# Kernel tuning notes

Measured on AMD Instinct MI355X. Metric: run time of the kernel, lower is better.

The kernel has to match this reference:

```python
import jax, jax.numpy as jnp
import numpy as np

NUM_HEADS = 8
NUM_GROUPS = 32
EPS = 1e-5


def setup_inputs() -> dict:
    key = jax.random.key(0)
    ks = jax.random.split(key, 7)
    B, C, H, W = 16, 512, 32, 32
    x = jax.random.normal(ks[0], (B, C, H, W), dtype=jnp.float32)
    gn_gamma = jnp.ones((C,), dtype=jnp.float32)
    gn_beta = jnp.zeros((C,), dtype=jnp.float32)
    # Conv1d with kernel_size=1 is a per-position matmul: weight [out, in]
    qkv_w = jax.random.normal(ks[1], (3 * C, C), dtype=jnp.float32) / np.sqrt(C)
    qkv_b = jax.random.normal(ks[2], (3 * C,), dtype=jnp.float32) * 0.01
    proj_w = jax.random.normal(ks[3], (C, C), dtype=jnp.float32) / np.sqrt(C)
    proj_b = jax.random.normal(ks[4], (C,), dtype=jnp.float32) * 0.01
    return {"x": x, "gn_gamma": gn_gamma, "gn_beta": gn_beta,
            "qkv_w": qkv_w, "qkv_b": qkv_b, "proj_w": proj_w, "proj_b": proj_b}


def group_norm(x, gamma, beta):
    # x: [B, C, H, W]
    B, C, H, W = x.shape
    xg = x.reshape(B, NUM_GROUPS, C // NUM_GROUPS, H, W)
    mean = xg.mean(axis=(2, 3, 4), keepdims=True)
    var = xg.var(axis=(2, 3, 4), keepdims=True)
    xg = (xg - mean) * jax.lax.rsqrt(var + EPS)
    x = xg.reshape(B, C, H, W)
    return x * gamma[None, :, None, None] + beta[None, :, None, None]


def reference(x, gn_gamma, gn_beta, qkv_w, qkv_b, proj_w, proj_b):
    B, C, H, W = x.shape
    N = H * W
    hd = C // NUM_HEADS  # head dim
    h = group_norm(x, gn_gamma, gn_beta).reshape(B, C, N)
    # 1x1 Conv1d == matmul over channel dim
    qkv = jnp.einsum('oc,bcn->bon', qkv_w, h) + qkv_b[None, :, None]
    qkv = qkv.reshape(B, 3, NUM_HEADS, hd, N)
    q, k, v = qkv[:, 0], qkv[:, 1], qkv[:, 2]  # each [B, h, d, N]
    scale = hd ** (-0.5)
    attn = jnp.einsum('bhdn,bhdm->bhnm', q, k) * scale  # [B, h, N, N]
    attn = jax.nn.softmax(attn, axis=-1)
    out = jnp.einsum('bhnm,bhdm->bhdn', attn, v).reshape(B, C, N)
    out = jnp.einsum('oc,bcn->bon', proj_w, out) + proj_b[None, :, None]
    return x + out.reshape(B, C, H, W)
```

## Files before the change

### kernel.cpp

```cpp
#include <hip/hip_runtime.h>

typedef unsigned short u16;
typedef unsigned int u32;
typedef __bf16 bf16x8 __attribute__((ext_vector_type(8)));
typedef float f32x4 __attribute__((ext_vector_type(4)));
typedef float f32x16 __attribute__((ext_vector_type(16)));

#define B_ 16
#define C_ 512
#define N_ 1024
#define NB_ 16384
#define K_ 512
#define M3_ 1536
#define SCALE_Q 0.18033688011112042f

__device__ __forceinline__ u16 f2bf(float f) {
  u32 u = __float_as_uint(f);
  u32 r = (u + 0x7FFFu + ((u >> 16) & 1u)) >> 16;
  return (u16)r;
}

__device__ __forceinline__ void gl_lds16(const void* g, void* l) {
  __builtin_amdgcn_global_load_lds(
      (const __attribute__((address_space(1))) u32*)(uintptr_t)g,
      (__attribute__((address_space(3))) u32*)(u32)(uintptr_t)l, 16, 0, 0);
}

__device__ __forceinline__ u32 cvtpk(float lo, float hi) {
  u32 r;
  asm("v_cvt_pk_bf16_f32 %0, %1, %2" : "=v"(r) : "v"(lo), "v"(hi));
  return r;
}

__device__ __forceinline__ float exp2a(float x) {
  float r;
  asm("v_exp_f32 %0, %1" : "=v"(r) : "v"(x));
  return r;
}

__device__ __forceinline__ void plswap2(u32& a, u32& b) {
#if __has_builtin(__builtin_amdgcn_permlane32_swap)
  auto r = __builtin_amdgcn_permlane32_swap((int)a, (int)b, false, false);
  a = (u32)r[0];
  b = (u32)r[1];
#else
  asm("v_permlane32_swap_b32 %0, %1" : "+v"(a), "+v"(b));
#endif
}

__device__ __forceinline__ float xhalf_sum(float x) {
  u32 a = __float_as_uint(x), b = a;
  plswap2(a, b);
  return __uint_as_float(a) + __uint_as_float(b);
}

__global__ __launch_bounds__(256) void cast2_kernel(const float* __restrict__ a,
                                                    const float* __restrict__ b,
                                                    u16* __restrict__ da,
                                                    u16* __restrict__ db,
                                                    int na, int nb) {
  int i = blockIdx.x * 256 + threadIdx.x;
  if (i < na) {
    da[i] = f2bf(a[i]);
  } else {
    int j = i - na;
    if (j < nb) db[j] = f2bf(b[j]);
  }
}

__global__ __launch_bounds__(256) void gnorm_kernel(const float* __restrict__ x,
                                                    const float* __restrict__ gamma,
                                                    const float* __restrict__ beta,
                                                    u16* __restrict__ ht) {
  int blk = blockIdx.x;
  int b = blk >> 5, g = blk & 31;
  int t = threadIdx.x;
  const float* xb = x + ((size_t)(b * C_ + g * 16) << 10);
  float v[16][4];
  float s = 0.f, sq = 0.f;
#pragma unroll
  for (int cc = 0; cc < 16; ++cc) {
#pragma unroll
    for (int r = 0; r < 4; ++r) {
      float f = xb[cc * 1024 + r * 256 + t];
      v[cc][r] = f; s += f; sq += f * f;
    }
  }
#pragma unroll
  for (int m = 32; m >= 1; m >>= 1) { s += __shfl_xor(s, m, 64); sq += __shfl_xor(sq, m, 64); }
  __shared__ float red[8];
  int w = t >> 6;
  if ((t & 63) == 0) { red[w * 2] = s; red[w * 2 + 1] = sq; }
  __syncthreads();
  s = red[0] + red[2] + red[4] + red[6];
  sq = red[1] + red[3] + red[5] + red[7];
  float mean = s * (1.f / 16384.f);
  float var = sq * (1.f / 16384.f) - mean * mean;
  float rstd = rsqrtf(var + 1e-5f);
  float gm[16], bt[16];
#pragma unroll
  for (int cc = 0; cc < 16; ++cc) {
    gm[cc] = gamma[g * 16 + cc] * rstd;
    bt[cc] = beta[g * 16 + cc];
  }
  u16* hb = ht + ((size_t)(b << 10)) * C_ + g * 16;
#pragma unroll
  for (int r = 0; r < 4; ++r) {
    u32 pk[8];
#pragma unroll
    for (int q = 0; q < 8; ++q) {
      float f0 = (v[2 * q][r] - mean) * gm[2 * q] + bt[2 * q];
      float f1 = (v[2 * q + 1][r] - mean) * gm[2 * q + 1] + bt[2 * q + 1];
      pk[q] = (u32)f2bf(f0) | ((u32)f2bf(f1) << 16);
    }
    u16* dp = hb + (size_t)(r * 256 + t) * C_;
    uint4 a = {pk[0], pk[1], pk[2], pk[3]};
    uint4 b4 = {pk[4], pk[5], pk[6], pk[7]};
    *(uint4*)dp = a;
    *(uint4*)(dp + 8) = b4;
  }
}

template <int EPI>
__global__ __launch_bounds__(256) void gemm_kernel(const u16* __restrict__ A,
                                                   const u16* __restrict__ BT,
                                                   const float* __restrict__ bias,
                                                   u16* __restrict__ Co,
                                                   u16* __restrict__ qTo,
                                                   u16* __restrict__ kTo,
                                                   const float* __restrict__ xres,
                                                   float* __restrict__ Fo) {
  __shared__ __attribute__((aligned(16))) u16 lds[4][8192];
  int t = threadIdx.x;
  int l = t & 63, w = t >> 6;
  int wr = w >> 1, wc = w & 1;
  int lid = blockIdx.y * 128 + blockIdx.x;
  int xcd = lid & 7, j2 = lid >> 3;
  int bx = xcd * 16 + (j2 & 15);
  int by = j2 >> 4;
  int ro0 = by * 128, co0 = bx * 128;
  f32x4 acc[4][4];
#pragma unroll
  for (int m = 0; m < 4; ++m)
#pragma unroll
    for (int n = 0; n < 4; ++n) acc[m][n] = {0.f, 0.f, 0.f, 0.f};

  int gsrc = ((l & 3) ^ ((l >> 3) & 3)) * 8;
  const u16* sA0 = A + (size_t)(ro0 + 2 * w * 16 + (l >> 2)) * K_ + gsrc;
  const u16* sA1 = sA0 + (size_t)16 * K_;
  const u16* sB0 = BT + (size_t)(co0 + 2 * w * 16 + (l >> 2)) * K_ + gsrc;
  const u16* sB1 = sB0 + (size_t)16 * K_;
  u32 dA0 = (2 * w) * 512, dA1 = (2 * w + 1) * 512;
  u32 dB0 = 4096 + (2 * w) * 512, dB1 = 4096 + (2 * w + 1) * 512;

  auto stage = [&](int hb) {
    u16* base = &lds[hb][0];
    gl_lds16(sA0, base + dA0);
    gl_lds16(sA1, base + dA1);
    gl_lds16(sB0, base + dB0);
    gl_lds16(sB1, base + dB1);
    sA0 += 32; sA1 += 32; sB0 += 32; sB1 += 32;
  };

  u32 slot = (((l >> 4) ^ (l >> 1)) & 3) * 8;
  u32 aro = (wr * 64 + (l & 15)) * 32 + slot;
  u32 bro = 4096 + (wc * 64 + (l & 15)) * 32 + slot;

  auto compute = [&](int hb) {
    const u16* base = &lds[hb][0];
    bf16x8 af[4], bfr[4];
#pragma unroll
    for (int m = 0; m < 4; ++m) af[m] = *(const bf16x8*)(base + aro + m * 512);
#pragma unroll
    for (int n = 0; n < 4; ++n) bfr[n] = *(const bf16x8*)(base + bro + n * 512);
    __builtin_amdgcn_s_setprio(1);
#pragma unroll
    for (int m = 0; m < 4; ++m)
#pragma unroll
      for (int n = 0; n < 4; ++n)
        acc[m][n] = __builtin_amdgcn_mfma_f32_16x16x32_bf16(af[m], bfr[n], acc[m][n], 0, 0, 0);
    __builtin_amdgcn_s_setprio(0);
  };

#define PHASE_SYNC(N)                                    \
  asm volatile("s_waitcnt vmcnt(" #N ")" ::: "memory"); \
  __builtin_amdgcn_sched_barrier(0);                     \
  __builtin_amdgcn_s_barrier();                          \
  __builtin_amdgcn_sched_barrier(0);

  stage(0);
  stage(1);
  stage(2);
#pragma unroll 1
  for (int h = 0; h < 13; ++h) {
    PHASE_SYNC(8)
    stage((h + 3) & 3);
    compute(h & 3);
  }
  PHASE_SYNC(8)
  compute(1);
  PHASE_SYNC(4)
  compute(2);
  PHASE_SYNC(0)
  compute(3);
#undef PHASE_SYNC

  if (EPI == 0 && ro0 < 1024) {
    int sel = ro0 >> 9;
    u16* dstb = sel ? kTo : qTo;
    float scl = sel ? 1.f : SCALE_Q;
#pragma unroll
    for (int m = 0; m < 4; ++m) {
      int row0 = ro0 + wr * 64 + m * 16 + (l >> 4) * 4;
      int o = row0 & 511;
      int h2 = o >> 6, d0 = o & 63;
      float bv0 = bias[row0], bv1 = bias[row0 + 1];
      float bv2 = bias[row0 + 2], bv3 = bias[row0 + 3];
#pragma unroll
      for (int n = 0; n < 4; ++n) {
        int col = co0 + wc * 64 + n * 16 + (l & 15);
        int bb = col >> 10, nn = col & 1023;
        float v0 = (acc[m][n][0] + bv0) * scl;
        float v1 = (acc[m][n][1] + bv1) * scl;
        float v2 = (acc[m][n][2] + bv2) * scl;
        float v3 = (acc[m][n][3] + bv3) * scl;
        uint2 ov = {cvtpk(v0, v1), cvtpk(v2, v3)};
        *(uint2*)(dstb + ((size_t)((bb * 8 + h2) << 10) + nn) * 64 + d0) = ov;
      }
    }
  } else {
#pragma unroll
    for (int m = 0; m < 4; ++m) {
#pragma unroll
      for (int j = 0; j < 4; ++j) {
        int row = ro0 + wr * 64 + m * 16 + (l >> 4) * 4 + j;
        float bv = bias[row];
#pragma unroll
        for (int n = 0; n < 4; ++n) {
          int col = co0 + wc * 64 + n * 16 + (l & 15);
          float val = acc[m][n][j] + bv;
          if (EPI == 0) {
            Co[(size_t)row * NB_ + col] = f2bf(val);
          } else {
            int bb = col >> 10, nn = col & 1023;
            size_t oi = (((size_t)(bb * C_ + row)) << 10) + nn;
            Fo[oi] = xres[oi] + val;
          }
        }
      }
    }
  }
}

__global__ __launch_bounds__(256) void attn_kernel(const u16* __restrict__ qT,
                                                   const u16* __restrict__ kT,
                                                   const u16* __restrict__ qkv,
                                                   u16* __restrict__ aoT) {
  __shared__ u16 KV[3][4096];
  int bid = blockIdx.x;
  int wid = (bid & 7) * 128 + (bid >> 3);
  int qt2 = wid & 7, h = (wid >> 3) & 7, b = wid >> 6;
  int bh = b * 8 + h;
  int t = threadIdx.x, l = t & 63, w = t >> 6;
  int lq = l & 31, hi = l >> 5;
  int q0 = qt2 * 128 + w * 32;

  const u16* qbase = qT + ((size_t)(bh << 10) + q0 + lq) * 64 + hi * 8;
  bf16x8 qf[4];
#pragma unroll
  for (int kc = 0; kc < 4; ++kc) qf[kc] = *(const bf16x8*)(qbase + kc * 16);

  f32x16 accO[2];
#pragma unroll
  for (int dt = 0; dt < 2; ++dt)
#pragma unroll
    for (int r = 0; r < 16; ++r) accO[dt][r] = 0.f;
  float lsum = 0.f;

  const u16 *src0, *src1;
  u32 ldso0, ldso1;
  int adv;
  if (w < 2) {
    int i0 = 2 * w, i1 = 2 * w + 1;
    src0 = kT + ((size_t)(bh << 10) + i0 * 8 + (l >> 3)) * 64 + (((l & 7) ^ ((l >> 3) & 7)) * 8);
    src1 = kT + ((size_t)(bh << 10) + i1 * 8 + (l >> 3)) * 64 + (((l & 7) ^ ((l >> 3) & 7)) * 8);
    ldso0 = i0 * 512; ldso1 = i1 * 512;
    adv = 2048;
  } else {
    int j0 = 2 * (w - 2), j1 = 2 * (w - 2) + 1;
    src0 = qkv + (size_t)(2 * C_ + h * 64 + j0 * 16 + (l >> 2)) * NB_ + (b << 10) +
           (((l & 3) ^ ((l >> 3) & 3)) * 8);
    src1 = qkv + (size_t)(2 * C_ + h * 64 + j1 * 16 + (l >> 2)) * NB_ + (b << 10) +
           (((l & 3) ^ ((l >> 3) & 3)) * 8);
    ldso0 = 2048 + j0 * 512; ldso1 = 2048 + j1 * 512;
    adv = 32;
  }

  u32 kfo[4], vfo[4];
#pragma unroll
  for (int kc = 0; kc < 4; ++kc)
    kfo[kc] = lq * 64 + (((2 * kc + hi) ^ (lq & 7)) * 8);
#pragma unroll
  for (int dt = 0; dt < 2; ++dt)
#pragma unroll
    for (int kcc = 0; kcc < 2; ++kcc)
      vfo[dt * 2 + kcc] = 2048 + (dt * 32 + lq) * 32 + (((kcc * 2 + hi) ^ ((lq >> 1) & 3)) * 8);

  auto stageTo = [&](u16* buf) {
    gl_lds16(src0, buf + ldso0);
    gl_lds16(src1, buf + ldso1);
    src0 += adv;
    src1 += adv;
  };

  auto qk = [&](const u16* buf, f32x16& sc) {
    bf16x8 kf[4];
#pragma unroll
    for (int kc = 0; kc < 4; ++kc) kf[kc] = *(const bf16x8*)(buf + kfo[kc]);
#pragma unroll
    for (int r = 0; r < 16; ++r) sc[r] = 0.f;
    __builtin_amdgcn_s_setprio(1);
#pragma unroll
    for (int kc = 0; kc < 4; ++kc)
      sc = __builtin_amdgcn_mfma_f32_32x32x16_bf16(kf[kc], qf[kc], sc, 0, 0, 0);
    __builtin_amdgcn_s_setprio(0);
  };

  auto finish = [&](const u16* buf, f32x16& sc) {
    bf16x8 vf[4];
#pragma unroll
    for (int j = 0; j < 4; ++j) vf[j] = *(const bf16x8*)(buf + vfo[j]);
    float p0 = 0.f, p1 = 0.f, p2 = 0.f, p3 = 0.f;
#pragma unroll
    for (int r = 0; r < 4; ++r) {
      float e0 = exp2a(sc[4 * r + 0]);
      float e1 = exp2a(sc[4 * r + 1]);
      float e2 = exp2a(sc[4 * r + 2]);
      float e3 = exp2a(sc[4 * r + 3]);
      sc[4 * r + 0] = e0; sc[4 * r + 1] = e1;
      sc[4 * r + 2] = e2; sc[4 * r + 3] = e3;
      p0 += e0; p1 += e1; p2 += e2; p3 += e3;
    }
    lsum += (p0 + p1) + (p2 + p3);
    u32 pk[8];
#pragma unroll
    for (int p = 0; p < 8; ++p) pk[p] = cvtpk(sc[2 * p], sc[2 * p + 1]);
    u32 pfu[2][4];
#pragma unroll
    for (int cc = 0; cc < 2; ++cc) {
      u32 w0 = pk[cc * 4 + 0], w2 = pk[cc * 4 + 2];
      u32 w1 = pk[cc * 4 + 1], w3 = pk[cc * 4 + 3];
      plswap2(w0, w2);
      plswap2(w1, w3);
      pfu[cc][0] = w0; pfu[cc][1] = w1; pfu[cc][2] = w2; pfu[cc][3] = w3;
    }
    __builtin_amdgcn_s_setprio(1);
#pragma unroll
    for (int kcc = 0; kcc < 2; ++kcc)
#pragma unroll
      for (int dt = 0; dt < 2; ++dt) {
        union { u32 u[4]; bf16x8 v; } pf;
        pf.u[0] = pfu[kcc][0]; pf.u[1] = pfu[kcc][1];
        pf.u[2] = pfu[kcc][2]; pf.u[3] = pfu[kcc][3];
        accO[dt] = __builtin_amdgcn_mfma_f32_32x32x16_bf16(vf[dt * 2 + kcc], pf.v, accO[dt], 0, 0, 0);
      }
    __builtin_amdgcn_s_setprio(0);
  };

#define WAITBAR(N)                                       \
  asm volatile("s_waitcnt vmcnt(" #N ")" ::: "memory"); \
  __builtin_amdgcn_sched_barrier(0);                     \
  __builtin_amdgcn_s_barrier();                          \
  __builtin_amdgcn_sched_barrier(0);

  u16* pa = &KV[0][0];
  u16* pb = &KV[1][0];
  u16* pc = &KV[2][0];
  f32x16 scA, scB;

  stageTo(pa);
  stageTo(pb);
  WAITBAR(0)
  qk(pa, scA);

#pragma unroll 1
  for (int s = 0; s < 15; ++s) {
    WAITBAR(0)
    stageTo(pc);
    qk(pb, scB);
    finish(pa, scA);
    u16* tp = pa; pa = pb; pb = pc; pc = tp;
    WAITBAR(0)
    stageTo(pc);
    qk(pb, scA);
    finish(pa, scB);
    tp = pa; pa = pb; pb = pc; pc = tp;
  }
  WAITBAR(0)
  qk(pb, scB);
  finish(pa, scA);
  pa = pb;
  finish(pa, scB);
#undef WAITBAR

  float inv = 1.0f / xhalf_sum(lsum);
  u16* ob = aoT + ((size_t)((b << 10) + q0 + lq)) * C_ + h * 64;
#pragma unroll
  for (int dt = 0; dt < 2; ++dt)
#pragma unroll
    for (int rg = 0; rg < 4; ++rg) {
      int d0 = dt * 32 + rg * 8 + hi * 4;
      u32 w0 = cvtpk(accO[dt][rg * 4 + 0] * inv, accO[dt][rg * 4 + 1] * inv);
      u32 w1 = cvtpk(accO[dt][rg * 4 + 2] * inv, accO[dt][rg * 4 + 3] * inv);
      uint2 o = {w0, w1};
      *(uint2*)(ob + d0) = o;
    }
}

extern "C" void kernel_launch(void* const* d_in, const int* in_sizes, int n_in,
                              void* d_out, int out_size, void* d_ws, size_t ws_size,
                              hipStream_t stream) {
  const float* x = (const float*)d_in[0];
  const float* gamma = (const float*)d_in[1];
  const float* beta = (const float*)d_in[2];
  const float* qkv_w = (const float*)d_in[3];
  const float* qkv_b = (const float*)d_in[4];
  const float* proj_w = (const float*)d_in[5];
  const float* proj_b = (const float*)d_in[6];
  float* out = (float*)d_out;
  char* ws = (char*)d_ws;
  u16* wq = (u16*)(ws);
  u16* wp = (u16*)(ws + 1572864);
  u16* ht = (u16*)(ws + 2097152);
  u16* qkvo = (u16*)(ws + 18874368);
  u16* qT = (u16*)(ws + 69206016);
  u16* kT = (u16*)(ws + 85983232);
  u16* aoT = ht;

  cast2_kernel<<<4096, 256, 0, stream>>>(qkv_w, proj_w, wq, wp, M3_ * K_, C_ * K_);
  gnorm_kernel<<<512, 256, 0, stream>>>(x, gamma, beta, ht);
  gemm_kernel<0><<<dim3(128, 12), 256, 0, stream>>>(wq, ht, qkv_b, qkvo, qT, kT, nullptr, nullptr);
  attn_kernel<<<1024, 256, 0, stream>>>(qT, kT, qkvo, aoT);
  gemm_kernel<1><<<dim3(128, 4), 256, 0, stream>>>(wp, aoT, proj_b, nullptr, nullptr, nullptr, x, out);
}
```

Before: 123.9 us.

## Add dedicated QKV GEMM kernel with 128x256 tiles and triple-buffered LDS

Replaces the generic GEMM template for the QKV projection with a specialized kernel using a wider 128x256 output tile per block (64x12 grid instead of 128x12), so each B-operand load is reused across more rows. It uses a three-stage LDS ring with global_load_lds prefetch two stages ahead, synchronized with vmcnt waits and barriers. The larger tile raises register pressure (32 accumulator vectors per thread) and halves the block count, which may lower occupancy and wave-level parallelism.

After: 127.8 us. 3.2% more time.

```diff
diff --git a/kernel.cpp b/kernel.cpp
--- a/kernel.cpp
+++ b/kernel.cpp
@@ -118,6 +118,128 @@
     uint4 b4 = {pk[4], pk[5], pk[6], pk[7]};
     *(uint4*)dp = a;
     *(uint4*)(dp + 8) = b4;
+  }
+}
+
+__global__ __launch_bounds__(256) void gemm_qkv_kernel(const u16* __restrict__ A,
+                                                       const u16* __restrict__ BT,
+                                                       const float* __restrict__ bias,
+                                                       u16* __restrict__ Co,
+                                                       u16* __restrict__ qTo,
+                                                       u16* __restrict__ kTo) {
+  __shared__ __attribute__((aligned(16))) u16 lds[3][12288];
+  int t = threadIdx.x;
+  int l = t & 63, w = t >> 6;
+  int wr = w >> 1, wc = w & 1;
+  int lid = blockIdx.y * 64 + blockIdx.x;
+  int xcd = lid & 7, j2 = lid >> 3;
+  int bx = xcd * 8 + (j2 & 7);
+  int by = j2 >> 3;
+  int ro0 = by * 128, co0 = bx * 256;
+  f32x4 acc[4][8];
+#pragma unroll
+  for (int m = 0; m < 4; ++m)
+#pragma unroll
+    for (int n = 0; n < 8; ++n) acc[m][n] = {0.f, 0.f, 0.f, 0.f};
+
+  int gsrc = ((l & 3) ^ ((l >> 3) & 3)) * 8;
+  const u16* sA0 = A + (size_t)(ro0 + 32 * w + (l >> 2)) * K_ + gsrc;
+  const u16* sA1 = sA0 + (size_t)16 * K_;
+  const u16* sB0 = BT + (size_t)(co0 + 64 * w + (l >> 2)) * K_ + gsrc;
+  const u16* sB1 = sB0 + (size_t)16 * K_;
+  const u16* sB2 = sB0 + (size_t)32 * K_;
+  const u16* sB3 = sB0 + (size_t)48 * K_;
+  u32 dA0 = (2 * w) * 512, dA1 = (2 * w + 1) * 512;
+  u32 dB0 = 4096 + (4 * w) * 512, dB1 = dB0 + 512, dB2 = dB0 + 1024, dB3 = dB0 + 1536;
+
+  auto stage = [&](int hb) {
+    u16* base = &lds[hb][0];
+    gl_lds16(sA0, base + dA0);
+    gl_lds16(sA1, base + dA1);
+    gl_lds16(sB0, base + dB0);
+    gl_lds16(sB1, base + dB1);
+    gl_lds16(sB2, base + dB2);
+    gl_lds16(sB3, base + dB3);
+    sA0 += 32; sA1 += 32; sB0 += 32; sB1 += 32; sB2 += 32; sB3 += 32;
+  };
+
+  u32 slot = (((l >> 4) ^ (l >> 1)) & 3) * 8;
+  u32 aro = (wr * 64 + (l & 15)) * 32 + slot;
+  u32 bro = 4096 + (wc * 128 + (l & 15)) * 32 + slot;
+
+  auto compute = [&](int hb) {
+    const u16* base = &lds[hb][0];
+    bf16x8 af[4], bfr[8];
+#pragma unroll
+    for (int m = 0; m < 4; ++m) af[m] = *(const bf16x8*)(base + aro + m * 512);
+#pragma unroll
+    for (int n = 0; n < 8; ++n) bfr[n] = *(const bf16x8*)(base + bro + n * 512);
+    __builtin_amdgcn_s_setprio(1);
+#pragma unroll
+    for (int m = 0; m < 4; ++m)
+#pragma unroll
+      for (int n = 0; n < 8; ++n)
+        acc[m][n] = __builtin_amdgcn_mfma_f32_16x16x32_bf16(af[m], bfr[n], acc[m][n], 0, 0, 0);
+    __builtin_amdgcn_s_setprio(0);
+  };
+
+#define PHASE_SYNC(N)                                    \
+  asm volatile("s_waitcnt vmcnt(" #N ")" ::: "memory"); \
+  __builtin_amdgcn_sched_barrier(0);                     \
+  __builtin_amdgcn_s_barrier();                          \
+  __builtin_amdgcn_sched_barrier(0);
+
+  stage(0);
+  stage(1);
+#pragma unroll 1
+  for (int h = 0; h < 14; ++h) {
+    PHASE_SYNC(6)
+    stage((h + 2) % 3);
+    compute(h % 3);
+  }
+  PHASE_SYNC(6)
+  compute(2);
+  PHASE_SYNC(0)
+  compute(0);
+#undef PHASE_SYNC
+
+  if (ro0 < 1024) {
+    int sel = ro0 >> 9;
+    u16* dstb = sel ? kTo : qTo;
+    float scl = sel ? 1.f : SCALE_Q;
+#pragma unroll
+    for (int m = 0; m < 4; ++m) {
+      int row0 = ro0 + wr * 64 + m * 16 + (l >> 4) * 4;
+      int o = row0 & 511;
+      int h2 = o >> 6, d0 = o & 63;
+      float bv0 = bias[row0], bv1 = bias[row0 + 1];
+      float bv2 = bias[row0 + 2], bv3 = bias[row0 + 3];
+#pragma unroll
+      for (int n = 0; n < 8; ++n) {
+        int col = co0 + wc * 128 + n * 16 + (l & 15);
+        int bb = col >> 10, nn = col & 1023;
+        float v0 = (acc[m][n][0] + bv0) * scl;
+        float v1 = (acc[m][n][1] + bv1) * scl;
+        float v2 = (acc[m][n][2] + bv2) * scl;
+        float v3 = (acc[m][n][3] + bv3) * scl;
+        uint2 ov = {cvtpk(v0, v1), cvtpk(v2, v3)};
+        *(uint2*)(dstb + ((size_t)((bb * 8 + h2) << 10) + nn) * 64 + d0) = ov;
+      }
+    }
+  } else {
+#pragma unroll
+    for (int m = 0; m < 4; ++m) {
+#pragma unroll
+      for (int j = 0; j < 4; ++j) {
+        int row = ro0 + wr * 64 + m * 16 + (l >> 4) * 4 + j;
+        float bv = bias[row];
+#pragma unroll
+        for (int n = 0; n < 8; ++n) {
+          int col = co0 + wc * 128 + n * 16 + (l & 15);
+          Co[(size_t)row * NB_ + col] = f2bf(acc[m][n][j] + bv);
+        }
+      }
+    }
   }
 }
 
@@ -439,7 +561,7 @@
 
   cast2_kernel<<<4096, 256, 0, stream>>>(qkv_w, proj_w, wq, wp, M3_ * K_, C_ * K_);
   gnorm_kernel<<<512, 256, 0, stream>>>(x, gamma, beta, ht);
-  gemm_kernel<0><<<dim3(128, 12), 256, 0, stream>>>(wq, ht, qkv_b, qkvo, qT, kT, nullptr, nullptr);
+  gemm_qkv_kernel<<<dim3(64, 12), 256, 0, stream>>>(wq, ht, qkv_b, qkvo, qT, kT);
   attn_kernel<<<1024, 256, 0, stream>>>(qT, kT, qkvo, aoT);
   gemm_kernel<1><<<dim3(128, 4), 256, 0, stream>>>(wp, aoT, proj_b, nullptr, nullptr, nullptr, x, out);
 }
```

## Deepen attention K/V LDS pipeline to four buffers with partial vmcnt waits

Applied to the files above, without the earlier changes.

The attention kernel's shared K/V staging grows from three to four buffers, so loads run two tiles ahead of compute. Waits use partial vmcnt counts instead of draining all outstanding global-to-LDS loads before each step. The loop is unrolled by four with fixed buffer rotation, removing pointer swaps. This hides more global-load latency at the cost of extra LDS (32KB per block), which may reduce occupancy.

Measured after the change: 123.5 us. No clear change (-0.3%).

```diff
diff --git a/kernel.cpp b/kernel.cpp
--- a/kernel.cpp
+++ b/kernel.cpp
@@ -256,7 +256,7 @@
                                                    const u16* __restrict__ kT,
                                                    const u16* __restrict__ qkv,
                                                    u16* __restrict__ aoT) {
-  __shared__ u16 KV[3][4096];
+  __shared__ u16 KV[4][4096];
   int bid = blockIdx.x;
   int wid = (bid & 7) * 128 + (bid >> 3);
   int qt2 = wid & 7, h = (wid >> 3) & 7, b = wid >> 6;
@@ -373,34 +373,37 @@
   __builtin_amdgcn_s_barrier();                          \
   __builtin_amdgcn_sched_barrier(0);
 
-  u16* pa = &KV[0][0];
-  u16* pb = &KV[1][0];
-  u16* pc = &KV[2][0];
+  u16* B0 = &KV[0][0];
+  u16* B1 = &KV[1][0];
+  u16* B2 = &KV[2][0];
+  u16* B3 = &KV[3][0];
   f32x16 scA, scB;
 
-  stageTo(pa);
-  stageTo(pb);
+  stageTo(B0);
+  stageTo(B1);
+  stageTo(B2);
+  WAITBAR(4)
+  qk(B0, scA);
+
+  WAITBAR(2)
+  stageTo(B3);
+  qk(B1, scB);
+  finish(B0, scA);
+
+#pragma unroll 1
+  for (int j = 0; j < 7; ++j) {
+    WAITBAR(2) stageTo(B0); qk(B2, scA); finish(B1, scB);
+    WAITBAR(2) stageTo(B1); qk(B3, scB); finish(B2, scA);
+    WAITBAR(2) stageTo(B2); qk(B0, scA); finish(B3, scB);
+    WAITBAR(2) stageTo(B3); qk(B1, scB); finish(B0, scA);
+  }
+  WAITBAR(2)
+  qk(B2, scA);
+  finish(B1, scB);
   WAITBAR(0)
-  qk(pa, scA);
-
-#pragma unroll 1
-  for (int s = 0; s < 15; ++s) {
-    WAITBAR(0)
-    stageTo(pc);
-    qk(pb, scB);
-    finish(pa, scA);
-    u16* tp = pa; pa = pb; pb = pc; pc = tp;
-    WAITBAR(0)
-    stageTo(pc);
-    qk(pb, scA);
-    finish(pa, scB);
-    tp = pa; pa = pb; pb = pc; pc = tp;
-  }
-  WAITBAR(0)
-  qk(pb, scB);
-  finish(pa, scA);
-  pa = pb;
-  finish(pa, scB);
+  qk(B3, scB);
+  finish(B2, scA);
+  finish(B3, scB);
 #undef WAITBAR
 
   float inv = 1.0f / xhalf_sum(lsum);
```
